# Kernel tuning notes

Hardware: AMD Instinct MI355X
Metric: run time of the kernel (lower is better)

Reference implementation:

```python
import jax, jax.numpy as jnp
import numpy as np

B = 1
DEPTH = 2
DIM = 256
HEADS = 8
MLP = 1024
NUM_CLASS = 4
PATCHES = 512
N = PATCHES * (NUM_CLASS + 1)  # 2560
HD = DIM // HEADS


def setup_inputs() -> dict:
    key = jax.random.key(0)
    ks = jax.random.split(key, 8)
    s = lambda k, shape: jax.random.normal(k, shape, jnp.float32) * 0.02
    return {
        "x": jax.random.normal(ks[0], (B, N, DIM), jnp.float32),
        "mask": jax.random.randint(ks[1], (B, NUM_CLASS), 0, 2, jnp.int32),
        "ln1_g": jnp.ones((DEPTH, DIM), jnp.float32),
        "ln1_b": jnp.zeros((DEPTH, DIM), jnp.float32),
        "Wqkv": s(ks[2], (DEPTH, DIM, 3 * DIM)),  # qkv_bias=False
        "Wproj": s(ks[3], (DEPTH, DIM, DIM)),
        "bproj": jnp.zeros((DEPTH, DIM), jnp.float32),
        "ln2_g": jnp.ones((DEPTH, DIM), jnp.float32),
        "ln2_b": jnp.zeros((DEPTH, DIM), jnp.float32),
        "W1": s(ks[4], (DEPTH, DIM, MLP)),
        "b1": jnp.zeros((DEPTH, MLP), jnp.float32),
        "W2": s(ks[5], (DEPTH, MLP, DIM)),
        "b2": jnp.zeros((DEPTH, DIM), jnp.float32),
    }


def layer_norm(x, g, b, eps=1e-5):
    mu = jnp.mean(x, axis=-1, keepdims=True)
    var = jnp.var(x, axis=-1, keepdims=True)
    return (x - mu) * jax.lax.rsqrt(var + eps) * g + b


def build_mask(mask):
    # Vectorized equivalent of mask_gen_fusion: block-diagonal per modality,
    # fusion rows attend everything except columns of missing modalities.
    blk = jnp.arange(N) // PATCHES  # [N], values in 0..NUM_CLASS
    base = blk[:, None] == blk[None, :]  # block diagonal (incl. fusion block)
    fusion_row = blk == NUM_CLASS  # [N]
    col_fusion = blk == NUM_CLASS  # [N]
    mod_ok = mask[:, jnp.clip(blk, 0, NUM_CLASS - 1)] == 1  # [B, N]
    allowed = jnp.where(fusion_row[None, :, None],
                        col_fusion[None, None, :] | mod_ok[:, None, :],
                        base[None, :, :])
    return allowed  # [B, N, N] bool


def reference(x, mask, ln1_g, ln1_b, Wqkv, Wproj, bproj, ln2_g, ln2_b, W1, b1, W2, b2):
    allowed = build_mask(mask)  # [B, N, N]
    scale = HD ** -0.5
    attns = []
    for d in range(DEPTH):
        # MaskedResidual(MaskedPreNormDrop(MaskedAttention))
        h = layer_norm(x, ln1_g[d], ln1_b[d])
        qkv = (h @ Wqkv[d]).reshape(B, N, 3, HEADS, HD)
        q, k, v = jnp.transpose(qkv, (2, 0, 3, 1, 4))  # each [B, H, N, HD]
        scores = jnp.einsum('bhnd,bhmd->bhnm', q, k) * scale
        scores = jnp.where(allowed[:, None, :, :], scores, -jnp.inf)
        attn = jax.nn.softmax(scores, axis=-1)  # [B, H, N, N]
        o = jnp.einsum('bhnm,bhmd->bhnd', attn, v)
        o = jnp.transpose(o, (0, 2, 1, 3)).reshape(B, N, DIM)
        o = o @ Wproj[d] + bproj[d]
        x = x + o
        attns.append(attn)
        # Residual(PreNorm(FeedForward)); F.gelu is exact erf gelu
        h2 = layer_norm(x, ln2_g[d], ln2_b[d])
        ff = jax.nn.gelu(h2 @ W1[d] + b1[d], approximate=False) @ W2[d] + b2[d]
        x = x + ff
    return x, jnp.stack(attns)
```

## Files before the change

### kernel.cpp

```cpp
#include <hip/hip_runtime.h>

#define NTOK 2560
#define NN ((long)NTOK*NTOK)

typedef __attribute__((ext_vector_type(8))) short short8;
typedef __attribute__((ext_vector_type(4))) float f32x4;

__device__ __forceinline__ unsigned short f2bf(float f){
  union { float f; unsigned int u; } v; v.f = f;
  unsigned int u = v.u + 0x7fffu + ((v.u >> 16) & 1u);
  return (unsigned short)(u >> 16);
}

__device__ __forceinline__ f32x4 mfma16(short8 a, short8 b, f32x4 c){
  return __builtin_amdgcn_mfma_f32_16x16x32_bf16(a, b, c, 0, 0, 0);
}

__global__ __launch_bounds__(256) void wt_all_k(
    const float* __restrict__ Wqkv, const float* __restrict__ Wproj,
    const float* __restrict__ W1, const float* __restrict__ W2,
    unsigned short* __restrict__ wqkvt, unsigned short* __restrict__ wprojt,
    unsigned short* __restrict__ w1t, unsigned short* __restrict__ w2t)
{
  __shared__ unsigned short T[64][68];
  int j = blockIdx.x;
  int d = j >= 192; j -= d*192;
  const float* src; unsigned short* dst; int K, N, tk, tn;
  if (j < 48){        src = Wqkv  + d*196608; dst = wqkvt  + d*196608; K=256;  N=768;  tk=j/12; tn=j-tk*12; }
  else if (j < 64){   j-=48;  src = Wproj + d*65536;  dst = wprojt + d*65536;  K=256;  N=256;  tk=j>>2; tn=j&3; }
  else if (j < 128){  j-=64;  src = W1    + d*262144; dst = w1t    + d*262144; K=256;  N=1024; tk=j>>4; tn=j&15; }
  else {              j-=128; src = W2    + d*262144; dst = w2t    + d*262144; K=1024; N=256;  tk=j>>2; tn=j&3; }
  int k0 = tk*64, n0 = tn*64;
  int r = threadIdx.x >> 2, c0 = (threadIdx.x & 3) * 16;
  const float* p = src + (long)(k0+r)*N + n0 + c0;
  #pragma unroll
  for (int e4 = 0; e4 < 4; e4++){
    f32x4 v = *(const f32x4*)(p + e4*4);
    #pragma unroll
    for (int e = 0; e < 4; e++) T[r][c0 + e4*4 + e] = f2bf(v[e]);
  }
  __syncthreads();
  unsigned short* q = dst + (long)(n0+r)*K + k0 + c0;
  short8 o0, o1;
  #pragma unroll
  for (int e = 0; e < 8; e++){ o0[e] = (short)T[c0+e][r]; o1[e] = (short)T[c0+8+e][r]; }
  *(short8*)q = o0;
  *(short8*)(q+8) = o1;
}

template<int EPI, bool LN>
__global__ __launch_bounds__(256) void gemm2_k(
    const void* __restrict__ Ap,
    const float* __restrict__ lng, const float* __restrict__ lnb,
    const unsigned short* __restrict__ Bt,
    int N, int K,
    const float* __restrict__ bias,
    const float* __restrict__ xin,
    float* __restrict__ xout,
    unsigned short* __restrict__ obf,
    unsigned short* __restrict__ qbf,
    unsigned short* __restrict__ kbf,
    unsigned short* __restrict__ vtbf)
{
  __shared__ __align__(16) unsigned short As[64][264];
  __shared__ __align__(16) unsigned short Bs[64][264];
  int tid = threadIdx.x, lane = tid & 63, w = tid >> 6;
  int wr = w >> 1, wc = w & 1;
  int m0 = blockIdx.y * 64, n0 = blockIdx.x * 64;
  int row = tid >> 2, q4 = tid & 3;
  int l15 = lane & 15;
  f32x4 acc[2][2] = {};

  for (int k0 = 0; k0 < K; k0 += 256){
    if (LN){
      const float* xrow = (const float*)Ap + (m0+row)*256;
      float s = 0.f, s2 = 0.f;
      #pragma unroll
      for (int j=0;j<8;j++){
        const float* p = xrow + (j*4+q4)*8;
        f32x4 va = *(const f32x4*)p;
        f32x4 vb = *(const f32x4*)(p+4);
        #pragma unroll
        for (int e=0;e<4;e++){ s += va[e]+vb[e]; s2 += va[e]*va[e]+vb[e]*vb[e]; }
      }
      s  += __shfl_xor(s, 1);  s2 += __shfl_xor(s2, 1);
      s  += __shfl_xor(s, 2);  s2 += __shfl_xor(s2, 2);
      float mu = s * (1.f/256.f);
      float inv = rsqrtf(s2*(1.f/256.f) - mu*mu + 1e-5f);
      #pragma unroll
      for (int j=0;j<8;j++){
        int c0 = (j*4+q4)*8;
        const float* p = xrow + c0;
        f32x4 va = *(const f32x4*)p;
        f32x4 vb = *(const f32x4*)(p+4);
        f32x4 ga = *(const f32x4*)&lng[c0], gb = *(const f32x4*)&lng[c0+4];
        f32x4 ba = *(const f32x4*)&lnb[c0], bb = *(const f32x4*)&lnb[c0+4];
        short8 o;
        #pragma unroll
        for (int e=0;e<4;e++){
          o[e]   = (short)f2bf((va[e]-mu)*inv*ga[e] + ba[e]);
          o[4+e] = (short)f2bf((vb[e]-mu)*inv*gb[e] + bb[e]);
        }
        *(short8*)&As[row][c0] = o;
      }
    } else {
      const unsigned short* Arow = (const unsigned short*)Ap + (long)(m0+row)*K + k0;
      #pragma unroll
      for (int j=0;j<8;j++){
        int c0 = (j*4+q4)*8;
        *(short8*)&As[row][c0] = *(const short8*)&Arow[c0];
      }
    }
    {
      const unsigned short* Brow = Bt + (long)(n0+row)*K + k0;
      #pragma unroll
      for (int j=0;j<8;j++){
        int c0 = (j*4+q4)*8;
        *(short8*)&Bs[row][c0] = *(const short8*)&Brow[c0];
      }
    }
    __syncthreads();
    #pragma unroll
    for (int ks=0; ks<8; ks++){
      int kc = ks*32 + (lane>>4)*8;
      short8 a0 = *(const short8*)&As[wr*32 + l15][kc];
      short8 a1 = *(const short8*)&As[wr*32 + 16 + l15][kc];
      short8 b0 = *(const short8*)&Bs[wc*32 + l15][kc];
      short8 b1 = *(const short8*)&Bs[wc*32 + 16 + l15][kc];
      acc[0][0] = mfma16(a0,b0,acc[0][0]);
      acc[0][1] = mfma16(a0,b1,acc[0][1]);
      acc[1][0] = mfma16(a1,b0,acc[1][0]);
      acc[1][1] = mfma16(a1,b1,acc[1][1]);
    }
    if (k0 + 256 < K) __syncthreads();
  }

  #pragma unroll
  for (int rt=0; rt<2; rt++)
  #pragma unroll
  for (int ct=0; ct<2; ct++)
  #pragma unroll
  for (int r=0; r<4; r++){
    int rg = m0 + wr*32 + rt*16 + (lane>>4)*4 + r;
    int cg = n0 + wc*32 + ct*16 + l15;
    float v = acc[rt][ct][r];
    if (EPI == 0){
      int which = cg >> 8, h = (cg >> 5) & 7, hd = cg & 31;
      if (which == 0)      qbf[(h*NTOK + rg)*32 + hd] = f2bf(v * 0.17677669529663687f);
      else if (which == 1) kbf[(h*NTOK + rg)*32 + hd] = f2bf(v);
      else                 vtbf[(h*32 + hd)*NTOK + rg] = f2bf(v);
    } else if (EPI == 1){
      xout[rg*N + cg] = xin[rg*N + cg] + v + bias[cg];
    } else {
      float t = v + bias[cg];
      float ge = 0.5f * t * (1.f + erff(t * 0.70710678118654752f));
      obf[rg*N + cg] = f2bf(ge);
    }
  }
}

__global__ __launch_bounds__(256) void attn_k(
    const unsigned short* __restrict__ qbf,
    const unsigned short* __restrict__ kbf,
    const unsigned short* __restrict__ vtbf,
    const int* __restrict__ mask,
    float* __restrict__ attn_out,
    unsigned short* __restrict__ obf)
{
  __shared__ __align__(16) float P32[32][268];
  __shared__ float O_red[4][32][32];
  __shared__ float reds[4][32];
  __shared__ float rowinv_s[32];

  int tid = threadIdx.x, lane = tid & 63, w = tid >> 6;
  int row0 = blockIdx.x * 32, h = blockIdx.y;
  int rblk = row0 >> 9;
  unsigned bits;
  if (rblk < 4) bits = 1u << rblk;
  else {
    bits = 16u;
    #pragma unroll
    for (int m=0; m<4; m++) if (mask[m] == 1) bits |= (1u << m);
  }
  int kk = (lane >> 4) * 8;
  int l15 = lane & 15;
  int rgrp = (lane >> 4) * 4;
  short8 aq0 = *(const short8*)&qbf[(h*NTOK + row0 + l15)*32 + kk];
  short8 aq1 = *(const short8*)&qbf[(h*NTOK + row0 + 16 + l15)*32 + kk];

  float s_[8] = {0,0,0,0,0,0,0,0};
  for (int b=0; b<5; b++){
    if (!((bits >> b) & 1)) continue;
    for (int ct=0; ct<8; ct++){
      int col = b*512 + w*128 + ct*16 + l15;
      short8 bk = *(const short8*)&kbf[(h*NTOK + col)*32 + kk];
      f32x4 s0 = {}; s0 = mfma16(aq0, bk, s0);
      f32x4 s1 = {}; s1 = mfma16(aq1, bk, s1);
      #pragma unroll
      for (int r=0;r<4;r++){ s_[r] += __expf(s0[r]); s_[4+r] += __expf(s1[r]); }
    }
  }
  #pragma unroll
  for (int msk=1; msk<16; msk<<=1)
    #pragma unroll
    for (int i=0;i<8;i++) s_[i] += __shfl_xor(s_[i], msk);
  if (l15 == 0){
    #pragma unroll
    for (int r=0;r<4;r++){ reds[w][rgrp + r] = s_[r]; reds[w][16 + rgrp + r] = s_[4+r]; }
  }
  __syncthreads();
  if (tid < 32) rowinv_s[tid] = 1.f / (reds[0][tid] + reds[1][tid] + reds[2][tid] + reds[3][tid]);
  __syncthreads();
  float rinv[8];
  #pragma unroll
  for (int r=0;r<4;r++){ rinv[r] = rowinv_s[rgrp + r]; rinv[4+r] = rowinv_s[16 + rgrp + r]; }

  f32x4 oacc[2][2] = {};
  for (int b=0; b<5; b++){
    long base = (long)h * NN + (long)row0 * NTOK + b*512;
    if ((bits >> b) & 1){
      #pragma unroll
      for (int hf=0; hf<2; hf++){
        #pragma unroll
        for (int ct=0; ct<4; ct++){
          int cl = w*64 + ct*16 + l15;
          short8 bk = *(const short8*)&kbf[(h*NTOK + b*512 + hf*256 + cl)*32 + kk];
          f32x4 s0 = {}; s0 = mfma16(aq0, bk, s0);
          f32x4 s1 = {}; s1 = mfma16(aq1, bk, s1);
          #pragma unroll
          for (int r=0;r<4;r++){
            P32[rgrp + r][cl]      = __expf(s0[r]) * rinv[r];
            P32[16 + rgrp + r][cl] = __expf(s1[r]) * rinv[4+r];
          }
        }
        __syncthreads();
        long hbase = base + hf*256;
        #pragma unroll
        for (int j=0;j<8;j++){
          int qi = j*256 + tid;
          int rl = qi >> 6, qc = (qi & 63) * 4;
          *(f32x4*)&attn_out[hbase + (long)rl*NTOK + qc] = *(const f32x4*)&P32[rl][qc];
        }
        #pragma unroll
        for (int ks2=0; ks2<2; ks2++){
          int kb = (w*2 + ks2)*32 + kk;
          f32x4 pa0a = *(const f32x4*)&P32[l15][kb],      pa0b = *(const f32x4*)&P32[l15][kb+4];
          f32x4 pa1a = *(const f32x4*)&P32[16 + l15][kb], pa1b = *(const f32x4*)&P32[16 + l15][kb+4];
          short8 pa0, pa1;
          #pragma unroll
          for (int e=0;e<4;e++){
            pa0[e] = (short)f2bf(pa0a[e]); pa0[4+e] = (short)f2bf(pa0b[e]);
            pa1[e] = (short)f2bf(pa1a[e]); pa1[4+e] = (short)f2bf(pa1b[e]);
          }
          #pragma unroll
          for (int hc=0; hc<2; hc++){
            short8 bv = *(const short8*)&vtbf[(h*32 + hc*16 + l15)*NTOK + b*512 + hf*256 + kb];
            oacc[0][hc] = mfma16(pa0, bv, oacc[0][hc]);
            oacc[1][hc] = mfma16(pa1, bv, oacc[1][hc]);
          }
        }
        __syncthreads();
      }
    } else {
      #pragma unroll
      for (int i=0;i<16;i++){
        int idx = tid + i*256;
        int rl = idx >> 7;
        int c4 = (idx & 127) << 2;
        f32x4 z = {0.f,0.f,0.f,0.f};
        *(f32x4*)&attn_out[base + (long)rl*NTOK + c4] = z;
      }
    }
  }
  #pragma unroll
  for (int rt=0; rt<2; rt++)
    #pragma unroll
    for (int hc=0; hc<2; hc++)
      #pragma unroll
      for (int r=0; r<4; r++)
        O_red[w][rt*16 + rgrp + r][hc*16 + l15] = oacc[rt][hc][r];
  __syncthreads();
  #pragma unroll
  for (int i2=0; i2<2; i2++){
    int i = tid + i2*256;
    int rl = i >> 4, c2 = (i & 15) * 2;
    float o0 = O_red[0][rl][c2]   + O_red[1][rl][c2]   + O_red[2][rl][c2]   + O_red[3][rl][c2];
    float o1 = O_red[0][rl][c2+1] + O_red[1][rl][c2+1] + O_red[2][rl][c2+1] + O_red[3][rl][c2+1];
    unsigned int pk = (unsigned int)f2bf(o0) | ((unsigned int)f2bf(o1) << 16);
    *(unsigned int*)&obf[(row0 + rl)*256 + h*32 + c2] = pk;
  }
}

extern "C" void kernel_launch(void* const* d_in, const int* in_sizes, int n_in,
                              void* d_out, int out_size, void* d_ws, size_t ws_size,
                              hipStream_t stream)
{
  const float* x_in  = (const float*)d_in[0];
  const int*   maskp = (const int*)d_in[1];
  const float* ln1g  = (const float*)d_in[2];
  const float* ln1b  = (const float*)d_in[3];
  const float* Wqkv  = (const float*)d_in[4];
  const float* Wproj = (const float*)d_in[5];
  const float* bproj = (const float*)d_in[6];
  const float* ln2g  = (const float*)d_in[7];
  const float* ln2b  = (const float*)d_in[8];
  const float* W1    = (const float*)d_in[9];
  const float* b1    = (const float*)d_in[10];
  const float* W2    = (const float*)d_in[11];
  const float* b2    = (const float*)d_in[12];
  float* out = (float*)d_out;

  char* ws = (char*)d_ws;
  float* x              = (float*)(ws + 0);
  unsigned short* mbf   = (unsigned short*)(ws + 2621440);
  unsigned short* obf   = (unsigned short*)(ws + 7864320);
  unsigned short* qbf   = (unsigned short*)(ws + 9175040);
  unsigned short* kbf   = (unsigned short*)(ws + 10485760);
  unsigned short* vtbf  = (unsigned short*)(ws + 11796480);
  unsigned short* wqkvt = (unsigned short*)(ws + 13107200);
  unsigned short* wprojt= (unsigned short*)(ws + 13893632);
  unsigned short* w1t   = (unsigned short*)(ws + 14155776);
  unsigned short* w2t   = (unsigned short*)(ws + 15204352);

  wt_all_k<<<384, 256, 0, stream>>>(Wqkv, Wproj, W1, W2, wqkvt, wprojt, w1t, w2t);

  for (int d=0; d<2; d++){
    const float* xsrc = d ? x : x_in;
    gemm2_k<0,true><<<dim3(12,40), 256, 0, stream>>>(xsrc, ln1g + d*256, ln1b + d*256,
        wqkvt + d*196608, 768, 256, nullptr, nullptr, nullptr, nullptr, qbf, kbf, vtbf);
    attn_k<<<dim3(80,8), 256, 0, stream>>>(qbf, kbf, vtbf, maskp,
        out + 655360 + (long)d*52428800, obf);
    gemm2_k<1,false><<<dim3(4,40), 256, 0, stream>>>(obf, nullptr, nullptr,
        wprojt + d*65536, 256, 256, bproj + d*256, xsrc, x, nullptr, nullptr, nullptr, nullptr);
    gemm2_k<2,true><<<dim3(16,40), 256, 0, stream>>>(x, ln2g + d*256, ln2b + d*256,
        w1t + d*262144, 1024, 256, b1 + d*1024, nullptr, nullptr, mbf, nullptr, nullptr, nullptr);
    float* xo = d ? out : x;
    gemm2_k<1,false><<<dim3(4,40), 256, 0, stream>>>(mbf, nullptr, nullptr,
        w2t + d*262144, 256, 1024, b2 + d*256, x, xo, nullptr, nullptr, nullptr, nullptr);
  }
}
```

Measured before the change: 196.7 us.

## Split attention probability writes into units overlapped with following GEMM launches

The attention kernel now computes only the output. It uses unnormalized exp values and applies the row normalization at the end, saving the per-row inverse sums to a workspace. Writing the full fp32 attention matrix is split into 3200 independent units. These run as extra blocks appended to the proj, MLP1 and MLP2 GEMM grids, plus a trailing kernel for the rest of layer 1. This removes the second QK pass and lets the bandwidth-bound attention writes overlap with GEMM compute. The cost is a much larger static shared-memory allocation in the GEMM kernel, which can limit occupancy, and more grid-partition bookkeeping.

```diff
diff --git a/kernel.cpp b/kernel.cpp
--- a/kernel.cpp
+++ b/kernel.cpp
@@ -46,6 +46,69 @@
   for (int e = 0; e < 8; e++){ o0[e] = (short)T[c0+e][r]; o1[e] = (short)T[c0+8+e][r]; }
   *(short8*)q = o0;
   *(short8*)(q+8) = o1;
+}
+
+__device__ __forceinline__ void p_unit_body(
+    int u, const unsigned short* __restrict__ qbf, const unsigned short* __restrict__ kbf,
+    const float* __restrict__ rinv_ws, float* __restrict__ attn_out,
+    const int* __restrict__ mask, char* smem)
+{
+  float (*P32)[268] = (float (*)[268])smem;
+  int tid = threadIdx.x, lane = tid & 63, w = tid >> 6;
+  int cb = u % 5, t2 = u / 5, tile = t2 % 80, h = t2 / 80;
+  int row0 = tile * 32;
+  int rblk = row0 >> 9;
+  unsigned bits;
+  if (rblk < 4) bits = 1u << rblk;
+  else {
+    bits = 16u;
+    #pragma unroll
+    for (int m=0; m<4; m++) if (mask[m]==1) bits |= (1u<<m);
+  }
+  long base = (long)h*NN + (long)row0*NTOK + cb*512;
+  if (!((bits >> cb) & 1)){
+    f32x4 z = {0.f,0.f,0.f,0.f};
+    #pragma unroll
+    for (int i=0;i<16;i++){
+      int idx = tid + i*256;
+      int rl = idx >> 7, c4 = (idx & 127) << 2;
+      *(f32x4*)&attn_out[base + (long)rl*NTOK + c4] = z;
+    }
+    return;
+  }
+  int kk = (lane>>4)*8, l15 = lane & 15, rgrp = (lane>>4)*4;
+  short8 aq0 = *(const short8*)&qbf[(h*NTOK + row0 + l15)*32 + kk];
+  short8 aq1 = *(const short8*)&qbf[(h*NTOK + row0 + 16 + l15)*32 + kk];
+  float rinv[8];
+  #pragma unroll
+  for (int r=0;r<4;r++){
+    rinv[r]   = rinv_ws[h*NTOK + row0 + rgrp + r];
+    rinv[4+r] = rinv_ws[h*NTOK + row0 + 16 + rgrp + r];
+  }
+  #pragma unroll
+  for (int hf=0; hf<2; hf++){
+    #pragma unroll
+    for (int ct=0; ct<4; ct++){
+      int cl = w*64 + ct*16 + l15;
+      short8 bk = *(const short8*)&kbf[(h*NTOK + cb*512 + hf*256 + cl)*32 + kk];
+      f32x4 s0 = {}; s0 = mfma16(aq0, bk, s0);
+      f32x4 s1 = {}; s1 = mfma16(aq1, bk, s1);
+      #pragma unroll
+      for (int r=0;r<4;r++){
+        P32[rgrp + r][cl]      = __expf(s0[r]) * rinv[r];
+        P32[16 + rgrp + r][cl] = __expf(s1[r]) * rinv[4+r];
+      }
+    }
+    __syncthreads();
+    long hbase = base + hf*256;
+    #pragma unroll
+    for (int j=0;j<8;j++){
+      int qi = j*256 + tid;
+      int rl = qi >> 6, qc = (qi & 63)*4;
+      *(f32x4*)&attn_out[hbase + (long)rl*NTOK + qc] = *(const f32x4*)&P32[rl][qc];
+    }
+    __syncthreads();
+  }
 }
 
 template<int EPI, bool LN>
@@ -60,10 +123,20 @@
     unsigned short* __restrict__ obf,
     unsigned short* __restrict__ qbf,
     unsigned short* __restrict__ kbf,
-    unsigned short* __restrict__ vtbf)
-{
-  __shared__ __align__(16) unsigned short As[64][264];
-  __shared__ __align__(16) unsigned short Bs[64][264];
+    unsigned short* __restrict__ vtbf,
+    int gx, int pbase,
+    const unsigned short* __restrict__ p_qbf, const unsigned short* __restrict__ p_kbf,
+    const float* __restrict__ p_rinv, float* __restrict__ p_attn,
+    const int* __restrict__ maskp)
+{
+  __shared__ __align__(16) char smem[135168];
+  if ((int)blockIdx.x >= gx){
+    int u = pbase + ((int)blockIdx.x - gx) * (int)gridDim.y + (int)blockIdx.y;
+    p_unit_body(u, p_qbf, p_kbf, p_rinv, p_attn, maskp, smem);
+    return;
+  }
+  unsigned short (*As)[264] = (unsigned short (*)[264])smem;
+  unsigned short (*Bs)[264] = (unsigned short (*)[264])(smem + 67584);
   int tid = threadIdx.x, lane = tid & 63, w = tid >> 6;
   int wr = w >> 1, wc = w & 1;
   int m0 = blockIdx.y * 64, n0 = blockIdx.x * 64;
@@ -159,12 +232,12 @@
   }
 }
 
-__global__ __launch_bounds__(256) void attn_k(
+__global__ __launch_bounds__(256) void attn_o_k(
     const unsigned short* __restrict__ qbf,
     const unsigned short* __restrict__ kbf,
     const unsigned short* __restrict__ vtbf,
     const int* __restrict__ mask,
-    float* __restrict__ attn_out,
+    float* __restrict__ rinv_ws,
     unsigned short* __restrict__ obf)
 {
   __shared__ __align__(16) float P32[32][268];
@@ -189,15 +262,45 @@
   short8 aq1 = *(const short8*)&qbf[(h*NTOK + row0 + 16 + l15)*32 + kk];
 
   float s_[8] = {0,0,0,0,0,0,0,0};
+  f32x4 oacc[2][2] = {};
   for (int b=0; b<5; b++){
     if (!((bits >> b) & 1)) continue;
-    for (int ct=0; ct<8; ct++){
-      int col = b*512 + w*128 + ct*16 + l15;
-      short8 bk = *(const short8*)&kbf[(h*NTOK + col)*32 + kk];
-      f32x4 s0 = {}; s0 = mfma16(aq0, bk, s0);
-      f32x4 s1 = {}; s1 = mfma16(aq1, bk, s1);
-      #pragma unroll
-      for (int r=0;r<4;r++){ s_[r] += __expf(s0[r]); s_[4+r] += __expf(s1[r]); }
+    #pragma unroll
+    for (int hf=0; hf<2; hf++){
+      #pragma unroll
+      for (int ct=0; ct<4; ct++){
+        int cl = w*64 + ct*16 + l15;
+        short8 bk = *(const short8*)&kbf[(h*NTOK + b*512 + hf*256 + cl)*32 + kk];
+        f32x4 s0 = {}; s0 = mfma16(aq0, bk, s0);
+        f32x4 s1 = {}; s1 = mfma16(aq1, bk, s1);
+        #pragma unroll
+        for (int r=0;r<4;r++){
+          float e0 = __expf(s0[r]), e1 = __expf(s1[r]);
+          s_[r] += e0; s_[4+r] += e1;
+          P32[rgrp + r][cl] = e0;
+          P32[16 + rgrp + r][cl] = e1;
+        }
+      }
+      __syncthreads();
+      #pragma unroll
+      for (int ks2=0; ks2<2; ks2++){
+        int kb = (w*2 + ks2)*32 + kk;
+        f32x4 pa0a = *(const f32x4*)&P32[l15][kb],      pa0b = *(const f32x4*)&P32[l15][kb+4];
+        f32x4 pa1a = *(const f32x4*)&P32[16 + l15][kb], pa1b = *(const f32x4*)&P32[16 + l15][kb+4];
+        short8 pa0, pa1;
+        #pragma unroll
+        for (int e=0;e<4;e++){
+          pa0[e] = (short)f2bf(pa0a[e]); pa0[4+e] = (short)f2bf(pa0b[e]);
+          pa1[e] = (short)f2bf(pa1a[e]); pa1[4+e] = (short)f2bf(pa1b[e]);
+        }
+        #pragma unroll
+        for (int hc=0; hc<2; hc++){
+          short8 bv = *(const short8*)&vtbf[(h*32 + hc*16 + l15)*NTOK + b*512 + hf*256 + kb];
+          oacc[0][hc] = mfma16(pa0, bv, oacc[0][hc]);
+          oacc[1][hc] = mfma16(pa1, bv, oacc[1][hc]);
+        }
+      }
+      __syncthreads();
     }
   }
   #pragma unroll
@@ -209,69 +312,12 @@
     for (int r=0;r<4;r++){ reds[w][rgrp + r] = s_[r]; reds[w][16 + rgrp + r] = s_[4+r]; }
   }
   __syncthreads();
-  if (tid < 32) rowinv_s[tid] = 1.f / (reds[0][tid] + reds[1][tid] + reds[2][tid] + reds[3][tid]);
+  if (tid < 32){
+    float inv = 1.f / (reds[0][tid] + reds[1][tid] + reds[2][tid] + reds[3][tid]);
+    rowinv_s[tid] = inv;
+    rinv_ws[h*NTOK + row0 + tid] = inv;
+  }
   __syncthreads();
-  float rinv[8];
-  #pragma unroll
-  for (int r=0;r<4;r++){ rinv[r] = rowinv_s[rgrp + r]; rinv[4+r] = rowinv_s[16 + rgrp + r]; }
-
-  f32x4 oacc[2][2] = {};
-  for (int b=0; b<5; b++){
-    long base = (long)h * NN + (long)row0 * NTOK + b*512;
-    if ((bits >> b) & 1){
-      #pragma unroll
-      for (int hf=0; hf<2; hf++){
-        #pragma unroll
-        for (int ct=0; ct<4; ct++){
-          int cl = w*64 + ct*16 + l15;
-          short8 bk = *(const short8*)&kbf[(h*NTOK + b*512 + hf*256 + cl)*32 + kk];
-          f32x4 s0 = {}; s0 = mfma16(aq0, bk, s0);
-          f32x4 s1 = {}; s1 = mfma16(aq1, bk, s1);
-          #pragma unroll
-          for (int r=0;r<4;r++){
-            P32[rgrp + r][cl]      = __expf(s0[r]) * rinv[r];
-            P32[16 + rgrp + r][cl] = __expf(s1[r]) * rinv[4+r];
-          }
-        }
-        __syncthreads();
-        long hbase = base + hf*256;
-        #pragma unroll
-        for (int j=0;j<8;j++){
-          int qi = j*256 + tid;
-          int rl = qi >> 6, qc = (qi & 63) * 4;
-          *(f32x4*)&attn_out[hbase + (long)rl*NTOK + qc] = *(const f32x4*)&P32[rl][qc];
-        }
-        #pragma unroll
-        for (int ks2=0; ks2<2; ks2++){
-          int kb = (w*2 + ks2)*32 + kk;
-          f32x4 pa0a = *(const f32x4*)&P32[l15][kb],      pa0b = *(const f32x4*)&P32[l15][kb+4];
-          f32x4 pa1a = *(const f32x4*)&P32[16 + l15][kb], pa1b = *(const f32x4*)&P32[16 + l15][kb+4];
-          short8 pa0, pa1;
-          #pragma unroll
-          for (int e=0;e<4;e++){
-            pa0[e] = (short)f2bf(pa0a[e]); pa0[4+e] = (short)f2bf(pa0b[e]);
-            pa1[e] = (short)f2bf(pa1a[e]); pa1[4+e] = (short)f2bf(pa1b[e]);
-          }
-          #pragma unroll
-          for (int hc=0; hc<2; hc++){
-            short8 bv = *(const short8*)&vtbf[(h*32 + hc*16 + l15)*NTOK + b*512 + hf*256 + kb];
-            oacc[0][hc] = mfma16(pa0, bv, oacc[0][hc]);
-            oacc[1][hc] = mfma16(pa1, bv, oacc[1][hc]);
-          }
-        }
-        __syncthreads();
-      }
-    } else {
-      #pragma unroll
-      for (int i=0;i<16;i++){
-        int idx = tid + i*256;
-        int rl = idx >> 7;
-        int c4 = (idx & 127) << 2;
-        f32x4 z = {0.f,0.f,0.f,0.f};
-        *(f32x4*)&attn_out[base + (long)rl*NTOK + c4] = z;
-      }
-    }
-  }
   #pragma unroll
   for (int rt=0; rt<2; rt++)
     #pragma unroll
@@ -284,11 +330,22 @@
   for (int i2=0; i2<2; i2++){
     int i = tid + i2*256;
     int rl = i >> 4, c2 = (i & 15) * 2;
-    float o0 = O_red[0][rl][c2]   + O_red[1][rl][c2]   + O_red[2][rl][c2]   + O_red[3][rl][c2];
-    float o1 = O_red[0][rl][c2+1] + O_red[1][rl][c2+1] + O_red[2][rl][c2+1] + O_red[3][rl][c2+1];
+    float inv = rowinv_s[rl];
+    float o0 = (O_red[0][rl][c2]   + O_red[1][rl][c2]   + O_red[2][rl][c2]   + O_red[3][rl][c2]) * inv;
+    float o1 = (O_red[0][rl][c2+1] + O_red[1][rl][c2+1] + O_red[2][rl][c2+1] + O_red[3][rl][c2+1]) * inv;
     unsigned int pk = (unsigned int)f2bf(o0) | ((unsigned int)f2bf(o1) << 16);
     *(unsigned int*)&obf[(row0 + rl)*256 + h*32 + c2] = pk;
   }
+}
+
+__global__ __launch_bounds__(256) void attn_p_k(
+    int pbase,
+    const unsigned short* __restrict__ qbf, const unsigned short* __restrict__ kbf,
+    const float* __restrict__ rinv_ws, float* __restrict__ attn_out,
+    const int* __restrict__ mask)
+{
+  __shared__ __align__(16) char smem[34304];
+  p_unit_body(pbase + blockIdx.x, qbf, kbf, rinv_ws, attn_out, mask, smem);
 }
 
 extern "C" void kernel_launch(void* const* d_in, const int* in_sizes, int n_in,
@@ -317,25 +374,33 @@
   unsigned short* qbf   = (unsigned short*)(ws + 9175040);
   unsigned short* kbf   = (unsigned short*)(ws + 10485760);
   unsigned short* vtbf  = (unsigned short*)(ws + 11796480);
-  unsigned short* wqkvt = (unsigned short*)(ws + 13107200);
-  unsigned short* wprojt= (unsigned short*)(ws + 13893632);
-  unsigned short* w1t   = (unsigned short*)(ws + 14155776);
-  unsigned short* w2t   = (unsigned short*)(ws + 15204352);
+  float* rinv           = (float*)(ws + 13107200);
+  unsigned short* wqkvt = (unsigned short*)(ws + 13238272);
+  unsigned short* wprojt= (unsigned short*)(ws + 14024704);
+  unsigned short* w1t   = (unsigned short*)(ws + 14286848);
+  unsigned short* w2t   = (unsigned short*)(ws + 15335424);
 
   wt_all_k<<<384, 256, 0, stream>>>(Wqkv, Wproj, W1, W2, wqkvt, wprojt, w1t, w2t);
 
   for (int d=0; d<2; d++){
     const float* xsrc = d ? x : x_in;
+    float* attn = out + 655360 + (long)d*52428800;
     gemm2_k<0,true><<<dim3(12,40), 256, 0, stream>>>(xsrc, ln1g + d*256, ln1b + d*256,
-        wqkvt + d*196608, 768, 256, nullptr, nullptr, nullptr, nullptr, qbf, kbf, vtbf);
-    attn_k<<<dim3(80,8), 256, 0, stream>>>(qbf, kbf, vtbf, maskp,
-        out + 655360 + (long)d*52428800, obf);
-    gemm2_k<1,false><<<dim3(4,40), 256, 0, stream>>>(obf, nullptr, nullptr,
-        wprojt + d*65536, 256, 256, bproj + d*256, xsrc, x, nullptr, nullptr, nullptr, nullptr);
-    gemm2_k<2,true><<<dim3(16,40), 256, 0, stream>>>(x, ln2g + d*256, ln2b + d*256,
-        w1t + d*262144, 1024, 256, b1 + d*1024, nullptr, nullptr, mbf, nullptr, nullptr, nullptr);
+        wqkvt + d*196608, 768, 256, nullptr, nullptr, nullptr, nullptr, qbf, kbf, vtbf,
+        12, 0, nullptr, nullptr, nullptr, nullptr, nullptr);
+    attn_o_k<<<dim3(80,8), 256, 0, stream>>>(qbf, kbf, vtbf, maskp, rinv, obf);
+    gemm2_k<1,false><<<dim3(24,40), 256, 0, stream>>>(obf, nullptr, nullptr,
+        wprojt + d*65536, 256, 256, bproj + d*256, xsrc, x, nullptr, nullptr, nullptr, nullptr,
+        4, 0, qbf, kbf, rinv, attn, maskp);
+    gemm2_k<2,true><<<dim3(46,40), 256, 0, stream>>>(x, ln2g + d*256, ln2b + d*256,
+        w1t + d*262144, 1024, 256, b1 + d*1024, nullptr, nullptr, mbf, nullptr, nullptr, nullptr,
+        16, 800, qbf, kbf, rinv, attn, maskp);
     float* xo = d ? out : x;
-    gemm2_k<1,false><<<dim3(4,40), 256, 0, stream>>>(mbf, nullptr, nullptr,
-        w2t + d*262144, 256, 1024, b2 + d*256, x, xo, nullptr, nullptr, nullptr, nullptr);
-  }
-}
+    int extra = d ? 20 : 30;
+    gemm2_k<1,false><<<dim3(4+extra,40), 256, 0, stream>>>(mbf, nullptr, nullptr,
+        w2t + d*262144, 256, 1024, b2 + d*256, x, xo, nullptr, nullptr, nullptr, nullptr,
+        4, 2000, qbf, kbf, rinv, attn, maskp);
+  }
+  attn_p_k<<<400, 256, 0, stream>>>(2800, qbf, kbf, rinv,
+      out + 655360 + (long)1*52428800, maskp);
+}
```

Result: no change. 196.7 us (-0.0%).

## Offload masked attention-zero writes into extra blocks of the GEMM kernels

Applied to the files above, without the earlier changes.

The attention kernel no longer writes zeros for masked-out attention blocks. That zero-fill work is split into units and handed to extra thread blocks appended to the four GEMM launches (QKV, proj, FC1, FC2). The aim is to overlap the large zero-store traffic with GEMMs that leave most of the GPU idle, and to shorten the attention kernel. The cost is larger GEMM grids and a shared-memory union, and correctness relies on the unit indexing covering every masked tile exactly once.

```diff
diff --git a/kernel.cpp b/kernel.cpp
--- a/kernel.cpp
+++ b/kernel.cpp
@@ -46,6 +46,32 @@
   for (int e = 0; e < 8; e++){ o0[e] = (short)T[c0+e][r]; o1[e] = (short)T[c0+8+e][r]; }
   *(short8*)q = o0;
   *(short8*)(q+8) = o1;
+}
+
+__device__ __forceinline__ void zero_unit_body(int u, const int* __restrict__ mask,
+                                               float* __restrict__ attn_out)
+{
+  int h = u / 320, rem = u - h*320;
+  int tile, cb;
+  if (rem < 256){
+    tile = rem >> 2;
+    int zi = rem & 3, rblk = tile >> 4;
+    cb = zi + (zi >= rblk);
+  } else {
+    int fz = rem - 256;
+    tile = 64 + (fz >> 2);
+    cb = fz & 3;
+    if (mask[cb] == 1) return;
+  }
+  long base = (long)h*NN + (long)tile*32*NTOK + cb*512;
+  f32x4 z = {0.f,0.f,0.f,0.f};
+  int tid = threadIdx.x;
+  #pragma unroll
+  for (int i=0;i<16;i++){
+    int idx = tid + i*256;
+    int rl = idx >> 7, c4 = (idx & 127) << 2;
+    *(f32x4*)&attn_out[base + (long)rl*NTOK + c4] = z;
+  }
 }
 
 template<int EPI, bool LN>
@@ -60,10 +86,18 @@
     unsigned short* __restrict__ obf,
     unsigned short* __restrict__ qbf,
     unsigned short* __restrict__ kbf,
-    unsigned short* __restrict__ vtbf)
-{
-  __shared__ __align__(16) unsigned short As[64][264];
-  __shared__ __align__(16) unsigned short Bs[64][264];
+    unsigned short* __restrict__ vtbf,
+    int gx, int zbase,
+    const int* __restrict__ maskp, float* __restrict__ p_attn)
+{
+  __shared__ __align__(16) char smem[67584];
+  if ((int)blockIdx.x >= gx){
+    int u = zbase + ((int)blockIdx.x - gx) * (int)gridDim.y + (int)blockIdx.y;
+    zero_unit_body(u, maskp, p_attn);
+    return;
+  }
+  unsigned short (*As)[264] = (unsigned short (*)[264])smem;
+  unsigned short (*Bs)[264] = (unsigned short (*)[264])(smem + 33792);
   int tid = threadIdx.x, lane = tid & 63, w = tid >> 6;
   int wr = w >> 1, wc = w & 1;
   int m0 = blockIdx.y * 64, n0 = blockIdx.x * 64;
@@ -159,7 +193,7 @@
   }
 }
 
-__global__ __launch_bounds__(256) void attn_k(
+__global__ __launch_bounds__(256) void attn_bk(
     const unsigned short* __restrict__ qbf,
     const unsigned short* __restrict__ kbf,
     const unsigned short* __restrict__ vtbf,
@@ -217,59 +251,49 @@
 
   f32x4 oacc[2][2] = {};
   for (int b=0; b<5; b++){
+    if (!((bits >> b) & 1)) continue;
     long base = (long)h * NN + (long)row0 * NTOK + b*512;
-    if ((bits >> b) & 1){
-      #pragma unroll
-      for (int hf=0; hf<2; hf++){
-        #pragma unroll
-        for (int ct=0; ct<4; ct++){
-          int cl = w*64 + ct*16 + l15;
-          short8 bk = *(const short8*)&kbf[(h*NTOK + b*512 + hf*256 + cl)*32 + kk];
-          f32x4 s0 = {}; s0 = mfma16(aq0, bk, s0);
-          f32x4 s1 = {}; s1 = mfma16(aq1, bk, s1);
-          #pragma unroll
-          for (int r=0;r<4;r++){
-            P32[rgrp + r][cl]      = __expf(s0[r]) * rinv[r];
-            P32[16 + rgrp + r][cl] = __expf(s1[r]) * rinv[4+r];
-          }
+    #pragma unroll
+    for (int hf=0; hf<2; hf++){
+      #pragma unroll
+      for (int ct=0; ct<4; ct++){
+        int cl = w*64 + ct*16 + l15;
+        short8 bk = *(const short8*)&kbf[(h*NTOK + b*512 + hf*256 + cl)*32 + kk];
+        f32x4 s0 = {}; s0 = mfma16(aq0, bk, s0);
+        f32x4 s1 = {}; s1 = mfma16(aq1, bk, s1);
+        #pragma unroll
+        for (int r=0;r<4;r++){
+          P32[rgrp + r][cl]      = __expf(s0[r]) * rinv[r];
+          P32[16 + rgrp + r][cl] = __expf(s1[r]) * rinv[4+r];
         }
-        __syncthreads();
-        long hbase = base + hf*256;
-        #pragma unroll
-        for (int j=0;j<8;j++){
-          int qi = j*256 + tid;
-          int rl = qi >> 6, qc = (qi & 63) * 4;
-          *(f32x4*)&attn_out[hbase + (long)rl*NTOK + qc] = *(const f32x4*)&P32[rl][qc];
+      }
+      __syncthreads();
+      long hbase = base + hf*256;
+      #pragma unroll
+      for (int j=0;j<8;j++){
+        int qi = j*256 + tid;
+        int rl = qi >> 6, qc = (qi & 63)*4;
+        *(f32x4*)&attn_out[hbase + (long)rl*NTOK + qc] = *(const f32x4*)&P32[rl][qc];
+      }
+      #pragma unroll
+      for (int ks2=0; ks2<2; ks2++){
+        int kb = (w*2 + ks2)*32 + kk;
+        f32x4 pa0a = *(const f32x4*)&P32[l15][kb],      pa0b = *(const f32x4*)&P32[l15][kb+4];
+        f32x4 pa1a = *(const f32x4*)&P32[16 + l15][kb], pa1b = *(const f32x4*)&P32[16 + l15][kb+4];
+        short8 pa0, pa1;
+        #pragma unroll
+        for (int e=0;e<4;e++){
+          pa0[e] = (short)f2bf(pa0a[e]); pa0[4+e] = (short)f2bf(pa0b[e]);
+          pa1[e] = (short)f2bf(pa1a[e]); pa1[4+e] = (short)f2bf(pa1b[e]);
         }
         #pragma unroll
-        for (int ks2=0; ks2<2; ks2++){
-          int kb = (w*2 + ks2)*32 + kk;
-          f32x4 pa0a = *(const f32x4*)&P32[l15][kb],      pa0b = *(const f32x4*)&P32[l15][kb+4];
-          f32x4 pa1a = *(const f32x4*)&P32[16 + l15][kb], pa1b = *(const f32x4*)&P32[16 + l15][kb+4];
-          short8 pa0, pa1;
-          #pragma unroll
-          for (int e=0;e<4;e++){
-            pa0[e] = (short)f2bf(pa0a[e]); pa0[4+e] = (short)f2bf(pa0b[e]);
-            pa1[e] = (short)f2bf(pa1a[e]); pa1[4+e] = (short)f2bf(pa1b[e]);
-          }
-          #pragma unroll
-          for (int hc=0; hc<2; hc++){
-            short8 bv = *(const short8*)&vtbf[(h*32 + hc*16 + l15)*NTOK + b*512 + hf*256 + kb];
-            oacc[0][hc] = mfma16(pa0, bv, oacc[0][hc]);
-            oacc[1][hc] = mfma16(pa1, bv, oacc[1][hc]);
-          }
+        for (int hc=0; hc<2; hc++){
+          short8 bv = *(const short8*)&vtbf[(h*32 + hc*16 + l15)*NTOK + b*512 + hf*256 + kb];
+          oacc[0][hc] = mfma16(pa0, bv, oacc[0][hc]);
+          oacc[1][hc] = mfma16(pa1, bv, oacc[1][hc]);
         }
-        __syncthreads();
-      }
-    } else {
-      #pragma unroll
-      for (int i=0;i<16;i++){
-        int idx = tid + i*256;
-        int rl = idx >> 7;
-        int c4 = (idx & 127) << 2;
-        f32x4 z = {0.f,0.f,0.f,0.f};
-        *(f32x4*)&attn_out[base + (long)rl*NTOK + c4] = z;
-      }
+      }
+      __syncthreads();
     }
   }
   #pragma unroll
@@ -326,16 +350,20 @@
 
   for (int d=0; d<2; d++){
     const float* xsrc = d ? x : x_in;
-    gemm2_k<0,true><<<dim3(12,40), 256, 0, stream>>>(xsrc, ln1g + d*256, ln1b + d*256,
-        wqkvt + d*196608, 768, 256, nullptr, nullptr, nullptr, nullptr, qbf, kbf, vtbf);
-    attn_k<<<dim3(80,8), 256, 0, stream>>>(qbf, kbf, vtbf, maskp,
-        out + 655360 + (long)d*52428800, obf);
-    gemm2_k<1,false><<<dim3(4,40), 256, 0, stream>>>(obf, nullptr, nullptr,
-        wprojt + d*65536, 256, 256, bproj + d*256, xsrc, x, nullptr, nullptr, nullptr, nullptr);
-    gemm2_k<2,true><<<dim3(16,40), 256, 0, stream>>>(x, ln2g + d*256, ln2b + d*256,
-        w1t + d*262144, 1024, 256, b1 + d*1024, nullptr, nullptr, mbf, nullptr, nullptr, nullptr);
+    float* attn = out + 655360 + (long)d*52428800;
+    gemm2_k<0,true><<<dim3(32,40), 256, 0, stream>>>(xsrc, ln1g + d*256, ln1b + d*256,
+        wqkvt + d*196608, 768, 256, nullptr, nullptr, nullptr, nullptr, qbf, kbf, vtbf,
+        12, 0, maskp, attn);
+    attn_bk<<<dim3(80,8), 256, 0, stream>>>(qbf, kbf, vtbf, maskp, attn, obf);
+    gemm2_k<1,false><<<dim3(20,40), 256, 0, stream>>>(obf, nullptr, nullptr,
+        wprojt + d*65536, 256, 256, bproj + d*256, xsrc, x, nullptr, nullptr, nullptr, nullptr,
+        4, 800, maskp, attn);
+    gemm2_k<2,true><<<dim3(32,40), 256, 0, stream>>>(x, ln2g + d*256, ln2b + d*256,
+        w1t + d*262144, 1024, 256, b1 + d*1024, nullptr, nullptr, mbf, nullptr, nullptr, nullptr,
+        16, 1440, maskp, attn);
     float* xo = d ? out : x;
-    gemm2_k<1,false><<<dim3(4,40), 256, 0, stream>>>(mbf, nullptr, nullptr,
-        w2t + d*262144, 256, 1024, b2 + d*256, x, xo, nullptr, nullptr, nullptr, nullptr);
-  }
-}
+    gemm2_k<1,false><<<dim3(16,40), 256, 0, stream>>>(mbf, nullptr, nullptr,
+        w2t + d*262144, 256, 1024, b2 + d*256, x, xo, nullptr, nullptr, nullptr, nullptr,
+        4, 2080, maskp, attn);
+  }
+}
```

Measured after the change: 238.9 us. 21.4% more time.
